# Kernel optimization log

Measured on AMD Instinct MI355X. Metric: run time of the kernel, lower is better.

The kernel has to match this reference:

```python
import jax, jax.numpy as jnp
import numpy as np

BLOCK = 32       # MX block size
EMAX_E4M3 = 8.0  # max exponent of fp8 e4m3 (max normal = 448 = 1.75 * 2^8)
NUM_HEADS = 16


def _e4m3_round(v):
    """Round values to fp8 e4m3 grid (bias 7, 3 mantissa bits, subnormals, max 448)."""
    absv = jnp.abs(v)
    e = jnp.floor(jnp.log2(jnp.where(absv > 0, absv, 1.0)))
    e = jnp.maximum(e, -6.0)                # min normal exponent; below -> subnormal grid
    step = jnp.exp2(e - 3.0)                # 3 mantissa bits
    q = jnp.round(v / step) * step          # round-half-even like IEEE
    q = jnp.clip(q, -448.0, 448.0)
    return jnp.where(absv > 0, q, jnp.zeros_like(q))


def _mx_quantize(x):
    """Blockwise (32 along last dim) shared-exponent (E8M0) fp8 e4m3 quant-dequant."""
    shp = x.shape
    xb = x.reshape(shp[:-1] + (shp[-1] // BLOCK, BLOCK))
    amax = jnp.max(jnp.abs(xb), axis=-1, keepdims=True)
    sexp = jnp.floor(jnp.log2(jnp.where(amax > 0, amax, 1.0))) - EMAX_E4M3
    sexp = jnp.clip(sexp, -127.0, 127.0)    # E8M0 scale range
    scale = jnp.where(amax > 0, jnp.exp2(sexp), jnp.ones_like(sexp))
    q = _e4m3_round(xb / scale) * scale
    return q.reshape(shp)


def mxq(x):
    return _mx_quantize(x)


def _mx_linear(x, W, b):
    # quantize activations and weights (blocks of 32 along the contraction dim)
    return jnp.einsum('bse,oe->bso', mxq(x), mxq(W)) + b


def setup_inputs() -> dict:
    key = jax.random.key(0)
    ks = jax.random.split(key, 9)
    B, S, E = 4, 1024, 1024
    inp = {
        'query': jax.random.normal(ks[0], (B, S, E), dtype=jnp.float32),
        'Wq': jax.random.normal(ks[1], (E, E), dtype=jnp.float32) * 0.02,
        'bq': jnp.zeros((E,), dtype=jnp.float32),
        'Wk': jax.random.normal(ks[2], (E, E), dtype=jnp.float32) * 0.02,
        'bk': jnp.zeros((E,), dtype=jnp.float32),
        'Wv': jax.random.normal(ks[3], (E, E), dtype=jnp.float32) * 0.02,
        'bv': jnp.zeros((E,), dtype=jnp.float32),
        'Wo': jax.random.normal(ks[4], (E, E), dtype=jnp.float32) * 0.02,
        'bo': jnp.zeros((E,), dtype=jnp.float32),
    }
    return inp


def reference(query, Wq, bq, Wk, bk, Wv, bv, Wo, bo):
    B, S, E = query.shape
    H = NUM_HEADS
    D = E // H
    Q = _mx_linear(query, Wq, bq).reshape(B, S, H, D).transpose(0, 2, 1, 3)
    K = _mx_linear(query, Wk, bk).reshape(B, S, H, D).transpose(0, 2, 1, 3)
    V = _mx_linear(query, Wv, bv).reshape(B, S, H, D).transpose(0, 2, 1, 3)
    scores = jnp.einsum('bhqd,bhkd->bhqk', Q, K) / jnp.sqrt(jnp.float32(D))
    scores = mxq(scores)                    # score quantizer (blocks of 32 along kv dim)
    attn = jax.nn.softmax(scores, axis=-1)  # dropout p=0 -> identity
    ctx = jnp.einsum('bhqk,bhkd->bhqd', attn, V)
    ctx = ctx.transpose(0, 2, 1, 3).reshape(B, S, E)
    return _mx_linear(ctx, Wo, bo)
```

## Files before the change

kernel.cpp:

```cpp
#include <hip/hip_runtime.h>
#include <hip/hip_bf16.h>
#include <cstdint>
#include <cstddef>


#define S_LEN 1024
#define E_DIM 1024
#define NH    16
#define DH    64
#define BATCH 4
#define NROWS (BATCH * S_LEN)

typedef short          bf16x8  __attribute__((ext_vector_type(8)));
typedef float          f32x4   __attribute__((ext_vector_type(4)));
typedef unsigned short u16x8   __attribute__((ext_vector_type(8)));
typedef unsigned short u16x4   __attribute__((ext_vector_type(4)));
typedef unsigned int   u32x4   __attribute__((ext_vector_type(4)));


__device__ __forceinline__ void mx_scale_bits(float amax, float& scale, float& inv) {
  int eb = (int)(__float_as_uint(amax) >> 23);
  int sb = eb - 8;
  sb = sb < 1 ? 1 : (sb > 253 ? 253 : sb);
  float sc = __uint_as_float((unsigned)sb << 23);
  float iv = __uint_as_float((unsigned)(254 - sb) << 23);
  bool nz = (amax > 0.0f);
  scale = nz ? sc : 1.0f;
  inv   = nz ? iv : 1.0f;
}

__device__ __forceinline__ void qdq2(float& a, float& b) {
  a = fminf(fmaxf(a, -448.0f), 448.0f);
  b = fminf(fmaxf(b, -448.0f), 448.0f);
  int p = __builtin_amdgcn_cvt_pk_fp8_f32(a, b, 0, false);
  a = __builtin_amdgcn_cvt_f32_fp8(p, 0);
  b = __builtin_amdgcn_cvt_f32_fp8(p, 1);
}

__device__ __forceinline__ unsigned short f32_to_bf16_rne(float f) {
  unsigned u = __float_as_uint(f);
  unsigned r = 0x7FFFu + ((u >> 16) & 1u);
  return (unsigned short)((u + r) >> 16);
}

__device__ __forceinline__ float quad_red_max(float x) {
  auto p = __builtin_amdgcn_permlane16_swap(__float_as_uint(x), __float_as_uint(x), false, false);
  x = fmaxf(__uint_as_float(p[0]), __uint_as_float(p[1]));
  auto q = __builtin_amdgcn_permlane32_swap(__float_as_uint(x), __float_as_uint(x), false, false);
  return fmaxf(__uint_as_float(q[0]), __uint_as_float(q[1]));
}
__device__ __forceinline__ float quad_red_min(float x) {
  auto p = __builtin_amdgcn_permlane16_swap(__float_as_uint(x), __float_as_uint(x), false, false);
  x = fminf(__uint_as_float(p[0]), __uint_as_float(p[1]));
  auto q = __builtin_amdgcn_permlane32_swap(__float_as_uint(x), __float_as_uint(x), false, false);
  return fminf(__uint_as_float(q[0]), __uint_as_float(q[1]));
}
__device__ __forceinline__ float quad_red_sum(float x) {
  auto p = __builtin_amdgcn_permlane16_swap(__float_as_uint(x), __float_as_uint(x), false, false);
  x = __uint_as_float(p[0]) + __uint_as_float(p[1]);
  auto q = __builtin_amdgcn_permlane32_swap(__float_as_uint(x), __float_as_uint(x), false, false);
  return __uint_as_float(q[0]) + __uint_as_float(q[1]);
}


__device__ __forceinline__ void mxq_body(const float* __restrict__ in,
                                         unsigned short* __restrict__ out, int b) {
  const float4* p = (const float4*)(in + (size_t)b * 32);
  float v[32];
#pragma unroll
  for (int g = 0; g < 8; ++g) {
    float4 t = p[g];
    v[g * 4 + 0] = t.x; v[g * 4 + 1] = t.y; v[g * 4 + 2] = t.z; v[g * 4 + 3] = t.w;
  }
  float amax = 0.0f;
#pragma unroll
  for (int i = 0; i < 32; ++i) amax = fmaxf(amax, __builtin_fabsf(v[i]));
  float scale, inv;
  mx_scale_bits(amax, scale, inv);
  u16x8* q = (u16x8*)(out + (size_t)b * 32);
#pragma unroll
  for (int g = 0; g < 4; ++g) {
    u16x8 o;
#pragma unroll
    for (int e = 0; e < 8; e += 2) {
      float a = v[g * 8 + e] * inv, c = v[g * 8 + e + 1] * inv;
      qdq2(a, c);
      o[e]     = (unsigned short)(__float_as_uint(a * scale) >> 16);
      o[e + 1] = (unsigned short)(__float_as_uint(c * scale) >> 16);
    }
    q[g] = o;
  }
}

__global__ __launch_bounds__(256)
void mxq_all(const float* __restrict__ x,
             const float* __restrict__ w0, const float* __restrict__ w1,
             const float* __restrict__ w2, const float* __restrict__ w3,
             unsigned short* __restrict__ ox,
             unsigned short* __restrict__ o0, unsigned short* __restrict__ o1,
             unsigned short* __restrict__ o2, unsigned short* __restrict__ o3) {
  int blk = blockIdx.x;
  const float* in;
  unsigned short* out;
  int base;
  if (blk < 512)      { in = x;  out = ox; base = blk; }
  else if (blk < 640) { in = w0; out = o0; base = blk - 512; }
  else if (blk < 768) { in = w1; out = o1; base = blk - 640; }
  else if (blk < 896) { in = w2; out = o2; base = blk - 768; }
  else                { in = w3; out = o3; base = blk - 896; }
  mxq_body(in, out, base * 256 + threadIdx.x);
}


__global__ __launch_bounds__(256)
void gemm_qkv(const unsigned short* __restrict__ XQ,
              const unsigned short* __restrict__ Wqw, const unsigned short* __restrict__ Wkw,
              const unsigned short* __restrict__ Wvw,
              const float* __restrict__ bq, const float* __restrict__ bk,
              const float* __restrict__ bv,
              unsigned short* __restrict__ Qhi, unsigned short* __restrict__ Qlo,
              unsigned short* __restrict__ Khi, unsigned short* __restrict__ Klo,
              unsigned short* __restrict__ Vthi, unsigned short* __restrict__ Vtlo) {
  const int z = blockIdx.z;
  const unsigned short* Bw = (z == 0) ? Wqw : (z == 1) ? Wkw : Wvw;
  const float* bias = (z == 0) ? bq : (z == 1) ? bk : bv;
  unsigned short* Phi = (z == 0) ? Qhi : (z == 1) ? Khi : Vthi;
  unsigned short* Plo = (z == 0) ? Qlo : (z == 1) ? Klo : Vtlo;
  const float pre = (z == 0) ? 0.125f : 1.0f;

  __shared__ unsigned short sA[2][128 * 64];
  __shared__ unsigned short sB[2][128 * 64];
  const int tid = threadIdx.x;
  const int w = tid >> 6, ln = tid & 63;
  const int fid = blockIdx.y * 8 + blockIdx.x;
  const int xcd = fid & 7, sq = fid >> 3;
  const int bm = (xcd * 4 + (sq & 3)) * 128, bn = (sq >> 2) * 128;
  const int wm = (w >> 1) * 64, wn = (w & 1) * 64;
  const int quad = ln >> 4, col = ln & 15;

  f32x4 acc[4][4];
  f32x4 zero = {0.0f, 0.0f, 0.0f, 0.0f};
#pragma unroll
  for (int i = 0; i < 4; ++i)
#pragma unroll
    for (int j = 0; j < 4; ++j) acc[i][j] = zero;

  const int srow = ln >> 3;
  const int gsw  = (ln & 7) ^ srow;
  const int xo0 = (quad ^ (ln & 7)) * 8;
  const int xo1 = ((quad ^ 4) ^ (ln & 7)) * 8;

  auto STAGE = [&](int bb, int k0) {
#pragma unroll
    for (int q = 0; q < 4; ++q) {
      int row = w * 32 + q * 8 + srow;
      const unsigned short* ga = XQ + (size_t)(bm + row) * 1024 + k0 + gsw * 8;
      const unsigned short* gb = Bw + (size_t)(bn + row) * 1024 + k0 + gsw * 8;
      __builtin_amdgcn_global_load_lds(
          (const __attribute__((address_space(1))) unsigned int*)ga,
          (__attribute__((address_space(3))) unsigned int*)(&sA[bb][0] + (w * 32 + q * 8) * 64),
          16, 0, 0);
      __builtin_amdgcn_global_load_lds(
          (const __attribute__((address_space(1))) unsigned int*)gb,
          (__attribute__((address_space(3))) unsigned int*)(&sB[bb][0] + (w * 32 + q * 8) * 64),
          16, 0, 0);
    }
  };

  STAGE(0, 0);
#pragma unroll 1
  for (int k0 = 0; k0 < 1024; k0 += 64) {
    const int cur = (k0 >> 6) & 1;
    if (k0 < 960) {
      STAGE(cur ^ 1, k0 + 64);
      asm volatile("s_waitcnt vmcnt(8)" ::: "memory");
    } else {
      asm volatile("s_waitcnt vmcnt(0)" ::: "memory");
    }
    __builtin_amdgcn_s_barrier();
    __builtin_amdgcn_sched_barrier(0);

    const unsigned short* pA = &sA[cur][0];
    const unsigned short* pB = &sB[cur][0];
#pragma unroll
    for (int ks = 0; ks < 2; ++ks) {
      const int xo = ks ? xo1 : xo0;
      bf16x8 af[4], bfr[4];
#pragma unroll
      for (int t = 0; t < 4; ++t) {
        af[t]  = *(const bf16x8*)(pA + (wm + t * 16 + col) * 64 + xo);
        bfr[t] = *(const bf16x8*)(pB + (wn + t * 16 + col) * 64 + xo);
      }
#pragma unroll
      for (int ti = 0; ti < 4; ++ti)
#pragma unroll
        for (int tj = 0; tj < 4; ++tj)
          acc[ti][tj] = __builtin_amdgcn_mfma_f32_16x16x32_bf16(af[ti], bfr[tj], acc[ti][tj], 0, 0, 0);
    }
    __builtin_amdgcn_sched_barrier(0);
    __builtin_amdgcn_s_barrier();
  }

#pragma unroll
  for (int ti = 0; ti < 4; ++ti) {
#pragma unroll
    for (int tj = 0; tj < 4; ++tj) {
      int n = bn + wn + tj * 16 + col;
      float bv_ = bias[n];
      if (z != 2) {
#pragma unroll
        for (int i = 0; i < 4; ++i) {
          int m = bm + wm + ti * 16 + quad * 4 + i;
          float v = (acc[ti][tj][i] + bv_) * pre;
          unsigned short h = f32_to_bf16_rne(v);
          float hf = __uint_as_float((unsigned)h << 16);
          Phi[(size_t)m * 1024 + n] = h;
          Plo[(size_t)m * 1024 + n] = f32_to_bf16_rne(v - hf);
        }
      } else {
        int m0 = bm + wm + ti * 16 + quad * 4;
        u16x4 h4, l4;
#pragma unroll
        for (int i = 0; i < 4; ++i) {
          float v = acc[ti][tj][i] + bv_;
          unsigned short h = f32_to_bf16_rne(v);
          float hf = __uint_as_float((unsigned)h << 16);
          h4[i] = h;
          l4[i] = f32_to_bf16_rne(v - hf);
        }
        size_t idx = ((size_t)((m0 >> 10) * 1024 + n)) * 1024 + (m0 & 1023);
        *(u16x4*)(Phi + idx) = h4;
        *(u16x4*)(Plo + idx) = l4;
      }
    }
  }
}


__global__ __launch_bounds__(256)
void gemm_o(const unsigned short* __restrict__ A, const unsigned short* __restrict__ Bw,
            const float* __restrict__ bias, float* __restrict__ C) {
  __shared__ unsigned short sA[2][64 * 64];
  __shared__ unsigned short sB[2][128 * 64];
  const int tid = threadIdx.x;
  const int w = tid >> 6, ln = tid & 63;
  const int fid = blockIdx.y * 8 + blockIdx.x;
  const int xcd = fid & 7, sq = fid >> 3;
  const int bm = (xcd * 8 + (sq & 7)) * 64, bn = (sq >> 3) * 128;
  const int wr = (w >> 1) * 32, wc = (w & 1) * 64;
  const int quad = ln >> 4, col = ln & 15;

  f32x4 acc[2][4];
  f32x4 zero = {0.0f, 0.0f, 0.0f, 0.0f};
#pragma unroll
  for (int i = 0; i < 2; ++i)
#pragma unroll
    for (int j = 0; j < 4; ++j) acc[i][j] = zero;

  const int srow = ln >> 3;
  const int gsw  = (ln & 7) ^ srow;
  const int xo0 = (quad ^ (ln & 7)) * 8;
  const int xo1 = ((quad ^ 4) ^ (ln & 7)) * 8;

  auto STAGE = [&](int bb, int k0) {
#pragma unroll
    for (int qa = 0; qa < 2; ++qa) {
      int row = w * 16 + qa * 8 + srow;
      __builtin_amdgcn_global_load_lds(
          (const __attribute__((address_space(1))) unsigned int*)(A + (size_t)(bm + row) * 1024 + k0 + gsw * 8),
          (__attribute__((address_space(3))) unsigned int*)(&sA[bb][0] + (w * 16 + qa * 8) * 64),
          16, 0, 0);
    }
#pragma unroll
    for (int qb = 0; qb < 4; ++qb) {
      int row = w * 32 + qb * 8 + srow;
      __builtin_amdgcn_global_load_lds(
          (const __attribute__((address_space(1))) unsigned int*)(Bw + (size_t)(bn + row) * 1024 + k0 + gsw * 8),
          (__attribute__((address_space(3))) unsigned int*)(&sB[bb][0] + (w * 32 + qb * 8) * 64),
          16, 0, 0);
    }
  };

  STAGE(0, 0);
#pragma unroll 1
  for (int k0 = 0; k0 < 1024; k0 += 64) {
    const int cur = (k0 >> 6) & 1;
    if (k0 < 960) {
      STAGE(cur ^ 1, k0 + 64);
      asm volatile("s_waitcnt vmcnt(6)" ::: "memory");
    } else {
      asm volatile("s_waitcnt vmcnt(0)" ::: "memory");
    }
    __builtin_amdgcn_s_barrier();
    __builtin_amdgcn_sched_barrier(0);

    const unsigned short* pA = &sA[cur][0];
    const unsigned short* pB = &sB[cur][0];
#pragma unroll
    for (int ks = 0; ks < 2; ++ks) {
      const int xo = ks ? xo1 : xo0;
      bf16x8 af[2], bfr[4];
#pragma unroll
      for (int t = 0; t < 2; ++t)
        af[t] = *(const bf16x8*)(pA + (wr + t * 16 + col) * 64 + xo);
#pragma unroll
      for (int t = 0; t < 4; ++t)
        bfr[t] = *(const bf16x8*)(pB + (wc + t * 16 + col) * 64 + xo);
#pragma unroll
      for (int ti = 0; ti < 2; ++ti)
#pragma unroll
        for (int tj = 0; tj < 4; ++tj)
          acc[ti][tj] = __builtin_amdgcn_mfma_f32_16x16x32_bf16(af[ti], bfr[tj], acc[ti][tj], 0, 0, 0);
    }
    __builtin_amdgcn_sched_barrier(0);
    __builtin_amdgcn_s_barrier();
  }

#pragma unroll
  for (int ti = 0; ti < 2; ++ti) {
#pragma unroll
    for (int tj = 0; tj < 4; ++tj) {
      int n = bn + wc + tj * 16 + col;
      float bv_ = bias[n];
#pragma unroll
      for (int i = 0; i < 4; ++i) {
        int m = bm + wr + ti * 16 + quad * 4 + i;
        C[(size_t)m * 1024 + n] = acc[ti][tj][i] + bv_;
      }
    }
  }
}


__global__ __launch_bounds__(256, 4)
void attn_kernel(const unsigned short* __restrict__ Qhi, const unsigned short* __restrict__ Qlo,
                 const unsigned short* __restrict__ Khi, const unsigned short* __restrict__ Klo,
                 const unsigned short* __restrict__ Vthi, const unsigned short* __restrict__ Vtlo,
                 unsigned short* __restrict__ ctxq) {
  const int tid = threadIdx.x;
  const int id = blockIdx.y * 16 + blockIdx.x;
  const int qt = (id >> 3) & 15;
  const int bh = ((id >> 7) << 3) | (id & 7);
  const int b = bh >> 4, h = bh & 15;
  const int w = tid >> 6, ln = tid & 63, quad = ln >> 4, col = ln & 15;

  __shared__ __align__(16) short sK[16384];

  bf16x8 qh[2], ql[2];
  {
    const size_t qoff = (size_t)(b * 1024 + qt * 64 + w * 16 + col) * 1024 + h * 64 + quad * 8;
    qh[0] = *(const bf16x8*)(Qhi + qoff);
    qh[1] = *(const bf16x8*)(Qhi + qoff + 32);
    ql[0] = *(const bf16x8*)(Qlo + qoff);
    ql[1] = *(const bf16x8*)(Qlo + qoff + 32);
  }

  const unsigned short* gplane = (w == 0) ? Khi : (w == 1) ? Klo : (w == 2) ? Vthi : Vtlo;
  short* splane = sK + w * 4096;
  const int r8 = ln >> 3;
  const int ch = (ln & 7) ^ r8;
  const unsigned short* bp = (w < 2)
      ? gplane + (size_t)(b * 1024 + r8) * 1024 + h * 64 + ch * 8
      : gplane + (size_t)(b * 1024 + h * 64 + r8) * 1024 + ch * 8;
  const int ktstep = (w < 2) ? 65536 : 64;

  const int xo0 = (quad ^ (col & 7)) * 8;
  const int xo1 = ((quad + 4) ^ (col & 7)) * 8;

  f32x4 o[4];
  f32x4 zero = {0.0f, 0.0f, 0.0f, 0.0f};
#pragma unroll
  for (int t = 0; t < 4; ++t) o[t] = zero;
  float m_ = -3.0e38f, l_ = 0.0f;

  const float LOG2E = 1.44269504088896340736f;

#pragma unroll 1
  for (int kt = 0; kt < 16; ++kt) {
    __syncthreads();
#pragma unroll
    for (int g = 0; g < 8; ++g) {
      __builtin_amdgcn_global_load_lds(
          (const __attribute__((address_space(1))) unsigned int*)(bp + g * 8192),
          (__attribute__((address_space(3))) unsigned int*)(splane + g * 512),
          16, 0, 0);
    }
    bp += ktstep;
    __syncthreads();

    f32x4 s[4];
#pragma unroll
    for (int t = 0; t < 4; ++t) s[t] = zero;
#pragma unroll
    for (int t = 0; t < 4; ++t) {
      const int rb = (t * 16 + col) * 64;
#pragma unroll
      for (int ks = 0; ks < 2; ++ks) {
        const int xo = ks ? xo1 : xo0;
        bf16x8 kh = *(const bf16x8*)(sK +        rb + xo);
        bf16x8 kl = *(const bf16x8*)(sK + 4096 + rb + xo);
        s[t] = __builtin_amdgcn_mfma_f32_16x16x32_bf16(kh, ql[ks], s[t], 0, 0, 0);
        s[t] = __builtin_amdgcn_mfma_f32_16x16x32_bf16(kl, qh[ks], s[t], 0, 0, 0);
        s[t] = __builtin_amdgcn_mfma_f32_16x16x32_bf16(kh, qh[ks], s[t], 0, 0, 0);
      }
    }

    float mx0 = fmaxf(fmaxf(fmaxf(s[0][0], s[0][1]), fmaxf(s[0][2], s[0][3])),
                      fmaxf(fmaxf(s[1][0], s[1][1]), fmaxf(s[1][2], s[1][3])));
    float mn0 = fminf(fminf(fminf(s[0][0], s[0][1]), fminf(s[0][2], s[0][3])),
                      fminf(fminf(s[1][0], s[1][1]), fminf(s[1][2], s[1][3])));
    float mx1 = fmaxf(fmaxf(fmaxf(s[2][0], s[2][1]), fmaxf(s[2][2], s[2][3])),
                      fmaxf(fmaxf(s[3][0], s[3][1]), fmaxf(s[3][2], s[3][3])));
    float mn1 = fminf(fminf(fminf(s[2][0], s[2][1]), fminf(s[2][2], s[2][3])),
                      fminf(fminf(s[3][0], s[3][1]), fminf(s[3][2], s[3][3])));
    mx0 = quad_red_max(mx0); mn0 = quad_red_min(mn0);
    mx1 = quad_red_max(mx1); mn1 = quad_red_min(mn1);

    float sc0, iv0, sc1, iv1;
    mx_scale_bits(fmaxf(mx0, -mn0), sc0, iv0);
    mx_scale_bits(fmaxf(mx1, -mn1), sc1, iv1);
    float scl0 = sc0 * LOG2E, scl1 = sc1 * LOG2E;
#pragma unroll
    for (int t = 0; t < 4; ++t) {
      float iv  = (t < 2) ? iv0 : iv1;
      float scl = (t < 2) ? scl0 : scl1;
      float q0 = s[t][0] * iv, q1 = s[t][1] * iv;
      qdq2(q0, q1);
      float q2 = s[t][2] * iv, q3 = s[t][3] * iv;
      qdq2(q2, q3);
      s[t][0] = q0 * scl; s[t][1] = q1 * scl;
      s[t][2] = q2 * scl; s[t][3] = q3 * scl;
    }
    float d0 = mx0 * iv0, d1 = mx1 * iv1;
    qdq2(d0, d1);
    float mt = fmaxf(d0 * scl0, d1 * scl1);

    if (__any(mt > m_ + 4.0f)) {
      float mnew  = fmaxf(m_, mt);
      float alpha = __builtin_amdgcn_exp2f(m_ - mnew);
      m_ = mnew;
      l_ *= alpha;
#pragma unroll
      for (int nt = 0; nt < 4; ++nt)
#pragma unroll
        for (int i = 0; i < 4; ++i) o[nt][i] *= alpha;
    }
#pragma unroll
    for (int t = 0; t < 4; ++t) {
      float p0 = __builtin_amdgcn_exp2f(s[t][0] - m_);
      float p1 = __builtin_amdgcn_exp2f(s[t][1] - m_);
      float p2 = __builtin_amdgcn_exp2f(s[t][2] - m_);
      float p3 = __builtin_amdgcn_exp2f(s[t][3] - m_);
      s[t][0] = p0; s[t][1] = p1; s[t][2] = p2; s[t][3] = p3;
      l_ += (p0 + p1) + (p2 + p3);
    }

    unsigned Wh[4][2], Wl[4][2];
#pragma unroll
    for (int t = 0; t < 4; ++t) {
#pragma unroll
      for (int u = 0; u < 2; ++u) {
        float a = s[t][2 * u], c = s[t][2 * u + 1];
        __hip_bfloat162 h2 = __float22bfloat162_rn(make_float2(a, c));
        unsigned uh = *(unsigned*)&h2;
        float af = __uint_as_float(uh << 16);
        float cf = __uint_as_float(uh & 0xffff0000u);
        __hip_bfloat162 l2 = __float22bfloat162_rn(make_float2(a - af, c - cf));
        Wh[t][u] = uh;
        Wl[t][u] = *(unsigned*)&l2;
      }
    }
    bf16x8 pah[2], pal[2];
#pragma unroll
    for (int ks = 0; ks < 2; ++ks) {
      auto a0  = __builtin_amdgcn_permlane32_swap(Wh[2 * ks][0], Wh[2 * ks + 1][0], false, false);
      auto j02 = __builtin_amdgcn_permlane16_swap(a0[0], a0[1], false, false);
      auto a1  = __builtin_amdgcn_permlane32_swap(Wh[2 * ks][1], Wh[2 * ks + 1][1], false, false);
      auto j13 = __builtin_amdgcn_permlane16_swap(a1[0], a1[1], false, false);
      u32x4 hw; hw[0] = j02[0]; hw[1] = j13[0]; hw[2] = j02[1]; hw[3] = j13[1];
      pah[ks] = __builtin_bit_cast(bf16x8, hw);
      auto b0  = __builtin_amdgcn_permlane32_swap(Wl[2 * ks][0], Wl[2 * ks + 1][0], false, false);
      auto k02 = __builtin_amdgcn_permlane16_swap(b0[0], b0[1], false, false);
      auto b1  = __builtin_amdgcn_permlane32_swap(Wl[2 * ks][1], Wl[2 * ks + 1][1], false, false);
      auto k13 = __builtin_amdgcn_permlane16_swap(b1[0], b1[1], false, false);
      u32x4 lw; lw[0] = k02[0]; lw[1] = k13[0]; lw[2] = k02[1]; lw[3] = k13[1];
      pal[ks] = __builtin_bit_cast(bf16x8, lw);
    }

#pragma unroll
    for (int nt = 0; nt < 4; ++nt) {
      const int rb = (nt * 16 + col) * 64;
#pragma unroll
      for (int ks = 0; ks < 2; ++ks) {
        const int xo = ks ? xo1 : xo0;
        bf16x8 vh = *(const bf16x8*)(sK +  8192 + rb + xo);
        bf16x8 vl = *(const bf16x8*)(sK + 12288 + rb + xo);
        o[nt] = __builtin_amdgcn_mfma_f32_16x16x32_bf16(vh, pal[ks], o[nt], 0, 0, 0);
        o[nt] = __builtin_amdgcn_mfma_f32_16x16x32_bf16(vl, pah[ks], o[nt], 0, 0, 0);
        o[nt] = __builtin_amdgcn_mfma_f32_16x16x32_bf16(vh, pah[ks], o[nt], 0, 0, 0);
      }
    }
  }

  float linv = 1.0f / quad_red_sum(l_);
#pragma unroll
  for (int nt = 0; nt < 4; ++nt)
#pragma unroll
    for (int i = 0; i < 4; ++i) o[nt][i] *= linv;

  float am0 = 0.0f, am1 = 0.0f;
#pragma unroll
  for (int i = 0; i < 4; ++i) {
    am0 = fmaxf(am0, fmaxf(__builtin_fabsf(o[0][i]), __builtin_fabsf(o[1][i])));
    am1 = fmaxf(am1, fmaxf(__builtin_fabsf(o[2][i]), __builtin_fabsf(o[3][i])));
  }
  am0 = quad_red_max(am0);
  am1 = quad_red_max(am1);
  float sc0, iv0, sc1, iv1;
  mx_scale_bits(am0, sc0, iv0);
  mx_scale_bits(am1, sc1, iv1);

  const int tok = b * 1024 + qt * 64 + w * 16 + col;
  const size_t base = (size_t)tok * 1024 + h * 64 + quad * 4;
#pragma unroll
  for (int nt = 0; nt < 4; ++nt) {
    float iv = (nt < 2) ? iv0 : iv1;
    float sc = (nt < 2) ? sc0 : sc1;
    float q0 = o[nt][0] * iv, q1 = o[nt][1] * iv;
    qdq2(q0, q1);
    float q2 = o[nt][2] * iv, q3 = o[nt][3] * iv;
    qdq2(q2, q3);
    u16x4 h4;
    h4[0] = (unsigned short)(__float_as_uint(q0 * sc) >> 16);
    h4[1] = (unsigned short)(__float_as_uint(q1 * sc) >> 16);
    h4[2] = (unsigned short)(__float_as_uint(q2 * sc) >> 16);
    h4[3] = (unsigned short)(__float_as_uint(q3 * sc) >> 16);
    *(u16x4*)(ctxq + base + nt * 16) = h4;
  }
}


extern "C" void kernel_launch(void* const* d_in, const int* in_sizes, int n_in,
                              void* d_out, int out_size, void* d_ws, size_t ws_size,
                              hipStream_t stream) {
  (void)in_sizes; (void)n_in; (void)out_size; (void)ws_size;
  const float* x  = (const float*)d_in[0];
  const float* Wq = (const float*)d_in[1];
  const float* bq = (const float*)d_in[2];
  const float* Wk = (const float*)d_in[3];
  const float* bk = (const float*)d_in[4];
  const float* Wv = (const float*)d_in[5];
  const float* bv = (const float*)d_in[6];
  const float* Wo = (const float*)d_in[7];
  const float* bo = (const float*)d_in[8];

  char* wsb = (char*)d_ws;
  const size_t MB = (size_t)1 << 20;
  unsigned short* XQb   = (unsigned short*)(wsb + 0);
  unsigned short* WQb   = (unsigned short*)(wsb + 8 * MB);
  unsigned short* WKb   = (unsigned short*)(wsb + 10 * MB);
  unsigned short* WVb   = (unsigned short*)(wsb + 12 * MB);
  unsigned short* WOb   = (unsigned short*)(wsb + 14 * MB);
  unsigned short* Qhi   = (unsigned short*)(wsb + 16 * MB);
  unsigned short* Qlo   = (unsigned short*)(wsb + 24 * MB);
  unsigned short* Khi   = (unsigned short*)(wsb + 32 * MB);
  unsigned short* Klo   = (unsigned short*)(wsb + 40 * MB);
  unsigned short* Vthi  = (unsigned short*)(wsb + 48 * MB);
  unsigned short* Vtlo  = (unsigned short*)(wsb + 56 * MB);
  unsigned short* CTXQb = XQb;

  mxq_all<<<1024, 256, 0, stream>>>(x, Wq, Wk, Wv, Wo, XQb, WQb, WKb, WVb, WOb);

  dim3 qkvgrid(E_DIM / 128, NROWS / 128, 3);
  gemm_qkv<<<qkvgrid, 256, 0, stream>>>(XQb, WQb, WKb, WVb, bq, bk, bv,
                                        Qhi, Qlo, Khi, Klo, Vthi, Vtlo);

  dim3 agrid(16, 64);
  attn_kernel<<<agrid, 256, 0, stream>>>(Qhi, Qlo, Khi, Klo, Vthi, Vtlo, CTXQb);

  dim3 ogrid(E_DIM / 128, NROWS / 64);
  gemm_o<<<ogrid, 256, 0, stream>>>(CTXQb, WOb, bo, (float*)d_out);
}
```

Before: 222.2 us.

## Fuse Q/K/V projections into one GEMM sharing the activation tile

The QKV projection now runs as a single launch of 512-thread blocks. Each block stages one activation tile in LDS and multiplies it against the Wq, Wk and Wv tiles, keeping three sets of accumulators. This replaces the three-way z grid, which reloaded the activation tile once per projection. In the attention kernel, the softmax scale multiply is folded into an fma inside the exp2 argument. The fused GEMM needs about 128KB of LDS per block and launches only 256 blocks, so occupancy and latency hiding may suffer.

After: 218.2 us. No clear change (-1.8%).

```diff
diff --git a/kernel.cpp b/kernel.cpp
--- a/kernel.cpp
+++ b/kernel.cpp
@@ -112,7 +112,7 @@
 }
 
 
-__global__ __launch_bounds__(256)
+__global__ __launch_bounds__(512, 2)
 void gemm_qkv(const unsigned short* __restrict__ XQ,
               const unsigned short* __restrict__ Wqw, const unsigned short* __restrict__ Wkw,
               const unsigned short* __restrict__ Wvw,
@@ -121,29 +121,26 @@
               unsigned short* __restrict__ Qhi, unsigned short* __restrict__ Qlo,
               unsigned short* __restrict__ Khi, unsigned short* __restrict__ Klo,
               unsigned short* __restrict__ Vthi, unsigned short* __restrict__ Vtlo) {
-  const int z = blockIdx.z;
-  const unsigned short* Bw = (z == 0) ? Wqw : (z == 1) ? Wkw : Wvw;
-  const float* bias = (z == 0) ? bq : (z == 1) ? bk : bv;
-  unsigned short* Phi = (z == 0) ? Qhi : (z == 1) ? Khi : Vthi;
-  unsigned short* Plo = (z == 0) ? Qlo : (z == 1) ? Klo : Vtlo;
-  const float pre = (z == 0) ? 0.125f : 1.0f;
-
-  __shared__ unsigned short sA[2][128 * 64];
-  __shared__ unsigned short sB[2][128 * 64];
+  __shared__ unsigned short sA [2][128 * 64];
+  __shared__ unsigned short sBq[2][128 * 64];
+  __shared__ unsigned short sBk[2][128 * 64];
+  __shared__ unsigned short sBv[2][128 * 64];
   const int tid = threadIdx.x;
   const int w = tid >> 6, ln = tid & 63;
   const int fid = blockIdx.y * 8 + blockIdx.x;
   const int xcd = fid & 7, sq = fid >> 3;
   const int bm = (xcd * 4 + (sq & 3)) * 128, bn = (sq >> 2) * 128;
-  const int wm = (w >> 1) * 64, wn = (w & 1) * 64;
+  const int wm = (w & 3) * 32, wn = (w >> 2) * 64;
   const int quad = ln >> 4, col = ln & 15;
 
-  f32x4 acc[4][4];
+  f32x4 acc[3][2][4];
   f32x4 zero = {0.0f, 0.0f, 0.0f, 0.0f};
 #pragma unroll
-  for (int i = 0; i < 4; ++i)
-#pragma unroll
-    for (int j = 0; j < 4; ++j) acc[i][j] = zero;
+  for (int z = 0; z < 3; ++z)
+#pragma unroll
+    for (int i = 0; i < 2; ++i)
+#pragma unroll
+      for (int j = 0; j < 4; ++j) acc[z][i][j] = zero;
 
   const int srow = ln >> 3;
   const int gsw  = (ln & 7) ^ srow;
@@ -152,17 +149,26 @@
 
   auto STAGE = [&](int bb, int k0) {
 #pragma unroll
-    for (int q = 0; q < 4; ++q) {
-      int row = w * 32 + q * 8 + srow;
-      const unsigned short* ga = XQ + (size_t)(bm + row) * 1024 + k0 + gsw * 8;
-      const unsigned short* gb = Bw + (size_t)(bn + row) * 1024 + k0 + gsw * 8;
+    for (int j = 0; j < 2; ++j) {
+      const int rowb = j * 64 + w * 8;
+      const int row = rowb + srow;
+      const size_t goffA = (size_t)(bm + row) * 1024 + k0 + gsw * 8;
+      const size_t goffB = (size_t)(bn + row) * 1024 + k0 + gsw * 8;
       __builtin_amdgcn_global_load_lds(
-          (const __attribute__((address_space(1))) unsigned int*)ga,
-          (__attribute__((address_space(3))) unsigned int*)(&sA[bb][0] + (w * 32 + q * 8) * 64),
+          (const __attribute__((address_space(1))) unsigned int*)(XQ + goffA),
+          (__attribute__((address_space(3))) unsigned int*)(&sA[bb][0] + rowb * 64),
           16, 0, 0);
       __builtin_amdgcn_global_load_lds(
-          (const __attribute__((address_space(1))) unsigned int*)gb,
-          (__attribute__((address_space(3))) unsigned int*)(&sB[bb][0] + (w * 32 + q * 8) * 64),
+          (const __attribute__((address_space(1))) unsigned int*)(Wqw + goffB),
+          (__attribute__((address_space(3))) unsigned int*)(&sBq[bb][0] + rowb * 64),
+          16, 0, 0);
+      __builtin_amdgcn_global_load_lds(
+          (const __attribute__((address_space(1))) unsigned int*)(Wkw + goffB),
+          (__attribute__((address_space(3))) unsigned int*)(&sBk[bb][0] + rowb * 64),
+          16, 0, 0);
+      __builtin_amdgcn_global_load_lds(
+          (const __attribute__((address_space(1))) unsigned int*)(Wvw + goffB),
+          (__attribute__((address_space(3))) unsigned int*)(&sBv[bb][0] + rowb * 64),
           16, 0, 0);
     }
   };
@@ -180,57 +186,88 @@
     __builtin_amdgcn_s_barrier();
     __builtin_amdgcn_sched_barrier(0);
 
-    const unsigned short* pA = &sA[cur][0];
-    const unsigned short* pB = &sB[cur][0];
 #pragma unroll
     for (int ks = 0; ks < 2; ++ks) {
       const int xo = ks ? xo1 : xo0;
-      bf16x8 af[4], bfr[4];
-#pragma unroll
-      for (int t = 0; t < 4; ++t) {
-        af[t]  = *(const bf16x8*)(pA + (wm + t * 16 + col) * 64 + xo);
-        bfr[t] = *(const bf16x8*)(pB + (wn + t * 16 + col) * 64 + xo);
-      }
-#pragma unroll
-      for (int ti = 0; ti < 4; ++ti)
-#pragma unroll
-        for (int tj = 0; tj < 4; ++tj)
-          acc[ti][tj] = __builtin_amdgcn_mfma_f32_16x16x32_bf16(af[ti], bfr[tj], acc[ti][tj], 0, 0, 0);
+      bf16x8 af[2];
+#pragma unroll
+      for (int t = 0; t < 2; ++t)
+        af[t] = *(const bf16x8*)(&sA[cur][0] + (wm + t * 16 + col) * 64 + xo);
+      {
+        bf16x8 bfr[4];
+#pragma unroll
+        for (int t = 0; t < 4; ++t)
+          bfr[t] = *(const bf16x8*)(&sBq[cur][0] + (wn + t * 16 + col) * 64 + xo);
+#pragma unroll
+        for (int ti = 0; ti < 2; ++ti)
+#pragma unroll
+          for (int tj = 0; tj < 4; ++tj)
+            acc[0][ti][tj] = __builtin_amdgcn_mfma_f32_16x16x32_bf16(af[ti], bfr[tj], acc[0][ti][tj], 0, 0, 0);
+      }
+      {
+        bf16x8 bfr[4];
+#pragma unroll
+        for (int t = 0; t < 4; ++t)
+          bfr[t] = *(const bf16x8*)(&sBk[cur][0] + (wn + t * 16 + col) * 64 + xo);
+#pragma unroll
+        for (int ti = 0; ti < 2; ++ti)
+#pragma unroll
+          for (int tj = 0; tj < 4; ++tj)
+            acc[1][ti][tj] = __builtin_amdgcn_mfma_f32_16x16x32_bf16(af[ti], bfr[tj], acc[1][ti][tj], 0, 0, 0);
+      }
+      {
+        bf16x8 bfr[4];
+#pragma unroll
+        for (int t = 0; t < 4; ++t)
+          bfr[t] = *(const bf16x8*)(&sBv[cur][0] + (wn + t * 16 + col) * 64 + xo);
+#pragma unroll
+        for (int ti = 0; ti < 2; ++ti)
+#pragma unroll
+          for (int tj = 0; tj < 4; ++tj)
+            acc[2][ti][tj] = __builtin_amdgcn_mfma_f32_16x16x32_bf16(af[ti], bfr[tj], acc[2][ti][tj], 0, 0, 0);
+      }
     }
     __builtin_amdgcn_sched_barrier(0);
     __builtin_amdgcn_s_barrier();
   }
 
 #pragma unroll
-  for (int ti = 0; ti < 4; ++ti) {
-#pragma unroll
-    for (int tj = 0; tj < 4; ++tj) {
-      int n = bn + wn + tj * 16 + col;
-      float bv_ = bias[n];
-      if (z != 2) {
-#pragma unroll
-        for (int i = 0; i < 4; ++i) {
-          int m = bm + wm + ti * 16 + quad * 4 + i;
-          float v = (acc[ti][tj][i] + bv_) * pre;
-          unsigned short h = f32_to_bf16_rne(v);
-          float hf = __uint_as_float((unsigned)h << 16);
-          Phi[(size_t)m * 1024 + n] = h;
-          Plo[(size_t)m * 1024 + n] = f32_to_bf16_rne(v - hf);
+  for (int z = 0; z < 3; ++z) {
+    const float* bias = (z == 0) ? bq : (z == 1) ? bk : bv;
+    unsigned short* Phi = (z == 0) ? Qhi : (z == 1) ? Khi : Vthi;
+    unsigned short* Plo = (z == 0) ? Qlo : (z == 1) ? Klo : Vtlo;
+    const float pre = (z == 0) ? 0.125f : 1.0f;
+#pragma unroll
+    for (int ti = 0; ti < 2; ++ti) {
+#pragma unroll
+      for (int tj = 0; tj < 4; ++tj) {
+        int n = bn + wn + tj * 16 + col;
+        float bv_ = bias[n];
+        if (z != 2) {
+#pragma unroll
+          for (int i = 0; i < 4; ++i) {
+            int m = bm + wm + ti * 16 + quad * 4 + i;
+            float v = (acc[z][ti][tj][i] + bv_) * pre;
+            unsigned short h = f32_to_bf16_rne(v);
+            float hf = __uint_as_float((unsigned)h << 16);
+            Phi[(size_t)m * 1024 + n] = h;
+            Plo[(size_t)m * 1024 + n] = f32_to_bf16_rne(v - hf);
+          }
+        } else {
+          int m0 = bm + wm + ti * 16 + quad * 4;
+          u16x4 h4, l4;
+#pragma unroll
+          for (int i = 0; i < 4; ++i) {
+            float v = acc[z][ti][tj][i] + bv_;
+            unsigned short h = f32_to_bf16_rne(v);
+            float hf = __uint_as_float((unsigned)h << 16);
+            h4[i] = h;
+            l4[i] = f32_to_bf16_rne(v - hf);
+          }
+          size_t idx = ((size_t)((m0 >> 10) * 1024 + n)) * 1024 + (m0 & 1023);
+          *(u16x4*)(Phi + idx) = h4;
+          *(u16x4*)(Plo + idx) = l4;
         }
-      } else {
-        int m0 = bm + wm + ti * 16 + quad * 4;
-        u16x4 h4, l4;
-#pragma unroll
-        for (int i = 0; i < 4; ++i) {
-          float v = acc[ti][tj][i] + bv_;
-          unsigned short h = f32_to_bf16_rne(v);
-          float hf = __uint_as_float((unsigned)h << 16);
-          h4[i] = h;
-          l4[i] = f32_to_bf16_rne(v - hf);
-        }
-        size_t idx = ((size_t)((m0 >> 10) * 1024 + n)) * 1024 + (m0 & 1023);
-        *(u16x4*)(Phi + idx) = h4;
-        *(u16x4*)(Plo + idx) = l4;
       }
     }
   }
@@ -422,14 +459,12 @@
     float scl0 = sc0 * LOG2E, scl1 = sc1 * LOG2E;
 #pragma unroll
     for (int t = 0; t < 4; ++t) {
-      float iv  = (t < 2) ? iv0 : iv1;
-      float scl = (t < 2) ? scl0 : scl1;
+      float iv = (t < 2) ? iv0 : iv1;
       float q0 = s[t][0] * iv, q1 = s[t][1] * iv;
       qdq2(q0, q1);
       float q2 = s[t][2] * iv, q3 = s[t][3] * iv;
       qdq2(q2, q3);
-      s[t][0] = q0 * scl; s[t][1] = q1 * scl;
-      s[t][2] = q2 * scl; s[t][3] = q3 * scl;
+      s[t][0] = q0; s[t][1] = q1; s[t][2] = q2; s[t][3] = q3;
     }
     float d0 = mx0 * iv0, d1 = mx1 * iv1;
     qdq2(d0, d1);
@@ -447,10 +482,11 @@
     }
 #pragma unroll
     for (int t = 0; t < 4; ++t) {
-      float p0 = __builtin_amdgcn_exp2f(s[t][0] - m_);
-      float p1 = __builtin_amdgcn_exp2f(s[t][1] - m_);
-      float p2 = __builtin_amdgcn_exp2f(s[t][2] - m_);
-      float p3 = __builtin_amdgcn_exp2f(s[t][3] - m_);
+      float scl = (t < 2) ? scl0 : scl1;
+      float p0 = __builtin_amdgcn_exp2f(__builtin_fmaf(s[t][0], scl, -m_));
+      float p1 = __builtin_amdgcn_exp2f(__builtin_fmaf(s[t][1], scl, -m_));
+      float p2 = __builtin_amdgcn_exp2f(__builtin_fmaf(s[t][2], scl, -m_));
+      float p3 = __builtin_amdgcn_exp2f(__builtin_fmaf(s[t][3], scl, -m_));
       s[t][0] = p0; s[t][1] = p1; s[t][2] = p2; s[t][3] = p3;
       l_ += (p0 + p1) + (p2 + p3);
     }
@@ -571,8 +607,8 @@
 
   mxq_all<<<1024, 256, 0, stream>>>(x, Wq, Wk, Wv, Wo, XQb, WQb, WKb, WVb, WOb);
 
-  dim3 qkvgrid(E_DIM / 128, NROWS / 128, 3);
-  gemm_qkv<<<qkvgrid, 256, 0, stream>>>(XQb, WQb, WKb, WVb, bq, bk, bv,
+  dim3 qkvgrid(8, 32);
+  gemm_qkv<<<qkvgrid, 512, 0, stream>>>(XQb, WQb, WKb, WVb, bq, bk, bv,
                                         Qhi, Qlo, Khi, Klo, Vthi, Vtlo);
 
   dim3 agrid(16, 64);
```
